# Performance work log

Hardware: AMD Instinct MI355X
Metric: run time of the kernel (lower is better)

## Reference

```python
import jax, jax.numpy as jnp
import numpy as np
import math

B, S, H, NH = 1, 2048, 1024, 16  # batch, seq, hidden, heads


def setup_inputs() -> dict:
    key = jax.random.key(0)
    ks = jax.random.split(key, 12)
    inp = {
        "query": jax.random.normal(ks[0], (B, S, H), dtype=jnp.float32),
        "key": jax.random.normal(ks[1], (B, S, H), dtype=jnp.float32),
        "value": jax.random.normal(ks[2], (B, S, H), dtype=jnp.float32),
        "attention_mask": jax.random.randint(ks[3], (1, 1, S, S), 0, 2, dtype=jnp.int32),
        # torch nn.Linear params: y = x @ W.T + b, W init ~ U(-1/sqrt(H), 1/sqrt(H))
        "Wq": jax.random.uniform(ks[4], (H, H), jnp.float32, -1, 1) / math.sqrt(H),
        "bq": jax.random.uniform(ks[5], (H,), jnp.float32, -1, 1) / math.sqrt(H),
        "Wk": jax.random.uniform(ks[6], (H, H), jnp.float32, -1, 1) / math.sqrt(H),
        "bk": jax.random.uniform(ks[7], (H,), jnp.float32, -1, 1) / math.sqrt(H),
        "Wv": jax.random.uniform(ks[8], (H, H), jnp.float32, -1, 1) / math.sqrt(H),
        "bv": jax.random.uniform(ks[9], (H,), jnp.float32, -1, 1) / math.sqrt(H),
        "Wo": jax.random.uniform(ks[10], (H, H), jnp.float32, -1, 1) / math.sqrt(H),
        "bo": jax.random.uniform(ks[11], (H,), jnp.float32, -1, 1) / math.sqrt(H),
        "head": NH,
        "hidden_size": H,
    }
    return inp


def reference(query, key, value, attention_mask, Wq, bq, Wk, bk, Wv, bv, Wo, bo, head, hidden_size):
    b, s, _ = query.shape
    d_k = hidden_size // head

    def proj(x, W, bias):
        # [b, s, hidden] -> [b, head, s, d_k]
        y = x @ W.T + bias
        return y.reshape(b, s, head, d_k).transpose(0, 2, 1, 3)

    q = proj(query, Wq, bq)
    k = proj(key, Wk, bk)
    v = proj(value, Wv, bv)

    # naive full score matrix, as in the source (scale by sqrt(d_k) = last dim of q)
    scores = jnp.einsum("bhqd,bhkd->bhqk", q, k) / math.sqrt(d_k)
    # faithful quirk: masked positions are set to 0 (not -inf) before softmax
    scores = jnp.where(attention_mask == 0, jnp.zeros((), scores.dtype), scores)
    attn = jax.nn.softmax(scores, axis=-1)

    out = jnp.einsum("bhqk,bhkd->bhqd", attn, v)  # [b, head, s, d_k]
    out = out.transpose(0, 2, 1, 3).reshape(b, s, head * d_k)
    return out @ Wo.T + bo
```

## Files before the change

kernel.cpp:

```cpp
#include <hip/hip_runtime.h>
#include <hip/hip_bf16.h>


#define S_LEN 2048
#define HID   1024
#define NHEAD 16
#define DK    64

typedef unsigned short u16;
typedef __attribute__((ext_vector_type(8))) short bf16x8;
typedef __attribute__((ext_vector_type(4))) short bf16x4;
typedef __attribute__((ext_vector_type(4))) float f32x4;

__device__ __forceinline__ void load16_lds(const void* g, void* l) {
  __builtin_amdgcn_global_load_lds(
      (const __attribute__((address_space(1))) void*)g,
      (__attribute__((address_space(3))) void*)l, 16, 0, 0);
}

__device__ __forceinline__ short bfbits(float x) {
  __hip_bfloat16 h = __float2bfloat16(x);
  return *(short*)&h;
}
__device__ __forceinline__ bf16x8 cvt8(float4 a, float4 b) {
  bf16x8 r;
  r[0] = bfbits(a.x); r[1] = bfbits(a.y); r[2] = bfbits(a.z); r[3] = bfbits(a.w);
  r[4] = bfbits(b.x); r[5] = bfbits(b.y); r[6] = bfbits(b.z); r[7] = bfbits(b.w);
  return r;
}
__device__ __forceinline__ float bf2f(u16 u) {
  unsigned v = (unsigned)u << 16;
  return *(float*)&v;
}

__global__ __launch_bounds__(256) void cvtW_kernel(
    const float* __restrict__ wq, const float* __restrict__ wk,
    const float* __restrict__ wv, const float* __restrict__ wo,
    u16* __restrict__ Wbf) {
  const int y = blockIdx.y;
  const float* src = y == 0 ? wq : (y == 1 ? wk : (y == 2 ? wv : wo));
  size_t i = ((size_t)blockIdx.x * 256 + threadIdx.x) * 8;
  float4 a = *(const float4*)(src + i);
  float4 b = *(const float4*)(src + i + 4);
  *(bf16x8*)(Wbf + (size_t)y * (HID * HID) + i) = cvt8(a, b);
}

__global__ void pack_mask_kernel(const int* __restrict__ mask,
                                 unsigned int* __restrict__ bits) {
  int w = blockIdx.x * blockDim.x + threadIdx.x;
  const int4* p = (const int4*)(mask + (size_t)w * 32);
  unsigned word = 0;
#pragma unroll
  for (int i = 0; i < 8; ++i) {
    int4 v = p[i];
    word |= (unsigned)(v.x != 0) << (i * 4 + 0);
    word |= (unsigned)(v.y != 0) << (i * 4 + 1);
    word |= (unsigned)(v.z != 0) << (i * 4 + 2);
    word |= (unsigned)(v.w != 0) << (i * 4 + 3);
  }
  bits[w] = word;
}

template <int BM, bool ABF>
__global__ __launch_bounds__(256) void gemm_bt(
    const void* A0, const void* A1, const void* A2,
    const u16* __restrict__ Wbase,
    const float* b0, const float* b1, const float* b2,
    void* C0, void* C1, void* C2,
    int store_fp32, int transpose_z2, int qscale_z0) {
  constexpr int Mm = 2048, Nn = 1024, Kk = 1024, BK = 64;
  constexpr int NIT = Kk / BK;
  constexpr int MT = BM / 32;
  constexpr int MTILES = Mm / BM;
  constexpr int AG = BM / 16;
  constexpr int AU = 2 * AG / 4;

  const int z = blockIdx.z;
  const void* A    = z == 0 ? A0 : (z == 1 ? A1 : A2);
  const u16*  W    = Wbase + (size_t)z * (Nn * Kk);
  const float* bias = z == 0 ? b0 : (z == 1 ? b1 : b2);
  void*       C    = z == 0 ? C0 : (z == 1 ? C1 : C2);
  const int transpose = (z == 2) ? transpose_z2 : 0;
  const float oscale = (z == 0 && qscale_z0) ? 0.125f : 1.0f;

  const int tid = threadIdx.x, lane = tid & 63, wave = tid >> 6;
  const int q4 = lane >> 4, c16 = lane & 15;
  const int bLin = blockIdx.x + blockIdx.y * gridDim.x;
  const int mBase = (bLin & (MTILES - 1)) * BM;
  const int nBase = (bLin / MTILES) * 128;
  const int wm = (wave >> 1) * (BM / 2), wn = (wave & 1) * 64;

  __shared__ __align__(16) u16 As[2][2][BM * 32];
  __shared__ __align__(16) u16 Bs[2][2][128 * 32];

  f32x4 acc[MT][4] = {};

  const int srow = lane >> 2;
  const int se8  = (lane & 3) * 8;

  const u16*   Ab = (const u16*)A;
  const float* Af = (const float*)A;

  auto issueW = [&](int it, int buf) {
#pragma unroll
    for (int j = 0; j < 4; ++j) {
      int i = wave * 4 + j;
      int h = i >> 3, grp = i & 7;
      load16_lds(W + (size_t)(nBase + grp * 16 + srow) * Kk + it * BK +
                     h * 32 + se8,
                 &Bs[buf][h][grp * 512]);
    }
  };
  auto issueA = [&](int it, int buf) {
#pragma unroll
    for (int j = 0; j < AU; ++j) {
      int i = wave * AU + j;
      int h = i / AG, grp = i % AG;
      load16_lds(Ab + (size_t)(mBase + grp * 16 + srow) * Kk + it * BK +
                     h * 32 + se8,
                 &As[buf][h][grp * 512]);
    }
  };
  float4 ar[AU][2];
  auto loadA = [&](int it) {
#pragma unroll
    for (int j = 0; j < AU; ++j) {
      int i = wave * AU + j;
      int h = i / AG, grp = i % AG;
      const float* s = Af + (size_t)(mBase + grp * 16 + srow) * Kk + it * BK +
                       h * 32 + se8;
      ar[j][0] = *(const float4*)s;
      ar[j][1] = *(const float4*)(s + 4);
    }
  };
  auto storeA = [&](int buf) {
#pragma unroll
    for (int j = 0; j < AU; ++j) {
      int i = wave * AU + j;
      int h = i / AG, grp = i % AG;
      *(bf16x8*)&As[buf][h][grp * 512 + srow * 32 + se8] =
          cvt8(ar[j][0], ar[j][1]);
    }
  };

  issueW(0, 0);
  if (ABF) {
    issueA(0, 0);
  } else {
    loadA(0);
    storeA(0);
  }
  __syncthreads();

  for (int it = 0; it < NIT; ++it) {
    const int buf = it & 1, nbuf = buf ^ 1;
    if (it + 1 < NIT) {
      issueW(it + 1, nbuf);
      if (ABF) issueA(it + 1, nbuf);
      else     loadA(it + 1);
    }
#pragma unroll
    for (int kk = 0; kk < 2; ++kk) {
      bf16x8 af[MT], bfr[4];
#pragma unroll
      for (int t = 0; t < MT; ++t)
        af[t] = *(const bf16x8*)&As[buf][kk][(wm + t * 16 + c16) * 32 + q4 * 8];
#pragma unroll
      for (int t = 0; t < 4; ++t)
        bfr[t] = *(const bf16x8*)&Bs[buf][kk][(wn + t * 16 + c16) * 32 + q4 * 8];
#pragma unroll
      for (int mt = 0; mt < MT; ++mt)
#pragma unroll
        for (int nt = 0; nt < 4; ++nt)
          acc[mt][nt] = __builtin_amdgcn_mfma_f32_16x16x32_bf16(
              af[mt], bfr[nt], acc[mt][nt], 0, 0, 0);
    }
    if (!ABF && it + 1 < NIT) storeA(nbuf);
    __syncthreads();
  }

#pragma unroll
  for (int nt = 0; nt < 4; ++nt) {
    int col = nBase + wn + nt * 16 + c16;
    float bv = bias[col];
#pragma unroll
    for (int mt = 0; mt < MT; ++mt) {
#pragma unroll
      for (int r = 0; r < 4; ++r) {
        int row = mBase + wm + mt * 16 + q4 * 4 + r;
        float v = (acc[mt][nt][r] + bv) * oscale;
        if (store_fp32)
          ((float*)C)[(size_t)row * Nn + col] = v;
        else if (transpose)
          ((__hip_bfloat16*)C)[(size_t)col * Mm + row] = __float2bfloat16(v);
        else
          ((__hip_bfloat16*)C)[(size_t)row * Nn + col] = __float2bfloat16(v);
      }
    }
  }
}

__global__ __launch_bounds__(256) void attn_kernel(
    const u16* __restrict__ Qb, const u16* __restrict__ Kb,
    const u16* __restrict__ Vt, const unsigned* __restrict__ mbits,
    u16* __restrict__ partO, float* __restrict__ partL) {
  constexpr int NITA = S_LEN / 2 / 64;
  const int qt = blockIdx.x, h = blockIdx.y, zz = blockIdx.z;
  const int tid = threadIdx.x, lane = tid & 63, wave = tid >> 6;
  const int q4 = lane >> 4, c16 = lane & 15;

  __shared__ __align__(16) u16 Ks[2][2][64 * 32];
  __shared__ __align__(16) u16 Vs[2][2][64 * 32];
  __shared__ __align__(16) u16 Ps[4][2 * 16 * 72];

  const int wq0 = qt * 128 + wave * 32;

  bf16x8 qf[2][2];
#pragma unroll
  for (int t = 0; t < 2; ++t)
#pragma unroll
    for (int kk = 0; kk < 2; ++kk)
      qf[t][kk] = *(const bf16x8*)(Qb + (size_t)(wq0 + t * 16 + c16) * HID +
                                   h * DK + kk * 32 + q4 * 8);

  f32x4 o[2][4] = {};
  float l_lane[2][4] = {};

  const int srow = lane >> 2;
  const int se8  = (lane & 3) * 8;
  const int kvbase = zz * (S_LEN / 2);

  auto issueKV = [&](int it, int buf) {
    const int kv0 = kvbase + it * 64;
#pragma unroll
    for (int j = 0; j < 2; ++j) {
      int ch = wave * 2 + j;
      int half = ch >> 2, grp = ch & 3;
      load16_lds(Kb + (size_t)(kv0 + grp * 16 + srow) * HID + h * DK +
                     half * 32 + se8,
                 &Ks[buf][half][grp * 512]);
      load16_lds(Vt + (size_t)(h * DK + grp * 16 + srow) * S_LEN + kv0 +
                     half * 32 + se8,
                 &Vs[buf][half][grp * 512]);
    }
  };

  issueKV(0, 0);
  __syncthreads();

  for (int it = 0; it < NITA; ++it) {
    const int buf = it & 1, nbuf = buf ^ 1;
    const int kv0 = kvbase + it * 64;
    if (it + 1 < NITA) issueKV(it + 1, nbuf);

    f32x4 sv[2][4];
#pragma unroll
    for (int nt = 0; nt < 4; ++nt) {
      bf16x8 kf0 = *(const bf16x8*)&Ks[buf][0][(nt * 16 + c16) * 32 + q4 * 8];
      bf16x8 kf1 = *(const bf16x8*)&Ks[buf][1][(nt * 16 + c16) * 32 + q4 * 8];
#pragma unroll
      for (int t = 0; t < 2; ++t) {
        f32x4 a = {};
        a = __builtin_amdgcn_mfma_f32_16x16x32_bf16(qf[t][0], kf0, a, 0, 0, 0);
        a = __builtin_amdgcn_mfma_f32_16x16x32_bf16(qf[t][1], kf1, a, 0, 0, 0);
        sv[t][nt] = a;
      }
    }

#pragma unroll
    for (int t = 0; t < 2; ++t)
#pragma unroll
      for (int r = 0; r < 4; ++r) {
        int row = wq0 + t * 16 + q4 * 4 + r;
        const unsigned* mrow = mbits + (size_t)row * 64 + (kv0 >> 5);
        unsigned w0 = mrow[0], w1 = mrow[1];
#pragma unroll
        for (int nt = 0; nt < 4; ++nt) {
          unsigned word = (nt < 2) ? w0 : w1;
          int bit = ((nt & 1) * 16) + c16;
          float s = ((word >> bit) & 1u) ? sv[t][nt][r] : 0.0f;
          float p = __expf(s);
          sv[t][nt][r] = p;
          l_lane[t][r] += p;
        }
      }

    u16* pw = &Ps[wave][0];
#pragma unroll
    for (int t = 0; t < 2; ++t)
#pragma unroll
      for (int r = 0; r < 4; ++r)
#pragma unroll
        for (int nt = 0; nt < 4; ++nt)
          ((__hip_bfloat16*)pw)[t * 1152 + (q4 * 4 + r) * 72 + nt * 16 + c16] =
              __float2bfloat16(sv[t][nt][r]);
    asm volatile("s_waitcnt lgkmcnt(0)" ::: "memory");

    bf16x8 vb[2][4];
#pragma unroll
    for (int kk = 0; kk < 2; ++kk)
#pragma unroll
      for (int nt = 0; nt < 4; ++nt)
        vb[kk][nt] =
            *(const bf16x8*)&Vs[buf][kk][(nt * 16 + c16) * 32 + q4 * 8];
#pragma unroll
    for (int t = 0; t < 2; ++t)
#pragma unroll
      for (int kk = 0; kk < 2; ++kk) {
        bf16x8 pa = *(const bf16x8*)&pw[t * 1152 + c16 * 72 + kk * 32 + q4 * 8];
#pragma unroll
        for (int nt = 0; nt < 4; ++nt)
          o[t][nt] = __builtin_amdgcn_mfma_f32_16x16x32_bf16(pa, vb[kk][nt],
                                                             o[t][nt], 0, 0, 0);
      }
    __syncthreads();
  }

#pragma unroll
  for (int t = 0; t < 2; ++t)
#pragma unroll
    for (int r = 0; r < 4; ++r) {
      float s = l_lane[t][r];
#pragma unroll
      for (int d = 1; d < 16; d <<= 1) s += __shfl_xor(s, d);
      l_lane[t][r] = s;
    }

#pragma unroll
  for (int t = 0; t < 2; ++t)
#pragma unroll
    for (int r = 0; r < 4; ++r) {
      int row = wq0 + t * 16 + q4 * 4 + r;
#pragma unroll
      for (int nt = 0; nt < 4; ++nt)
        ((__hip_bfloat16*)partO)[((size_t)zz * S_LEN + row) * HID + h * DK +
                                 nt * 16 + c16] = __float2bfloat16(o[t][nt][r]);
      if (c16 == 0)
        partL[((size_t)zz * NHEAD + h) * S_LEN + row] = l_lane[t][r];
    }
}

__global__ __launch_bounds__(256) void combine_kernel(
    const u16* __restrict__ partO, const float* __restrict__ partL,
    u16* __restrict__ ctx) {
  size_t idx = ((size_t)blockIdx.x * 256 + threadIdx.x) * 4;
  int row = (int)(idx >> 10);
  int col = (int)(idx & 1023);
  int h = col >> 6;
  float l = partL[(size_t)h * S_LEN + row] +
            partL[((size_t)NHEAD + h) * S_LEN + row];
  float inv = 1.0f / l;
  bf16x4 a = *(const bf16x4*)(partO + idx);
  bf16x4 b = *(const bf16x4*)(partO + (size_t)S_LEN * HID + idx);
  bf16x4 r;
#pragma unroll
  for (int j = 0; j < 4; ++j) {
    float v = (bf2f((u16)a[j]) + bf2f((u16)b[j])) * inv;
    r[j] = bfbits(v);
  }
  *(bf16x4*)(ctx + idx) = r;
}

extern "C" void kernel_launch(void* const* d_in, const int* in_sizes, int n_in,
                              void* d_out, int out_size, void* d_ws, size_t ws_size,
                              hipStream_t stream) {
  const float* q    = (const float*)d_in[0];
  const float* k    = (const float*)d_in[1];
  const float* v    = (const float*)d_in[2];
  const int*   mask = (const int*)d_in[3];
  const float* Wq = (const float*)d_in[4];
  const float* bq = (const float*)d_in[5];
  const float* Wk = (const float*)d_in[6];
  const float* bk = (const float*)d_in[7];
  const float* Wv = (const float*)d_in[8];
  const float* bv = (const float*)d_in[9];
  const float* Wo = (const float*)d_in[10];
  const float* bo = (const float*)d_in[11];

  const size_t M2 = (size_t)S_LEN * HID;
  const size_t need = (4 + 2 + 2 + 2 + 2) * M2 * 2 +
                      (size_t)S_LEN * 64 * 4 + 2 * NHEAD * S_LEN * 4;
  if (ws_size < need) return;

  u16* Wbf   = (u16*)d_ws;
  u16* partO = Wbf + 4 * (size_t)HID * HID / 2 * 2;
  u16* Qb    = partO + 2 * M2;
  u16* Kb    = Qb + M2;
  u16* Vt    = Kb + M2;
  unsigned* mbits = (unsigned*)(Vt + M2);
  float* partL = (float*)(mbits + (size_t)S_LEN * 64);
  u16* ctx = Qb;

  hipLaunchKernelGGL(cvtW_kernel, dim3(512, 4), dim3(256), 0, stream,
                     Wq, Wk, Wv, Wo, Wbf);

  hipLaunchKernelGGL(pack_mask_kernel, dim3((S_LEN * (S_LEN / 32)) / 256),
                     dim3(256), 0, stream, mask, mbits);

  hipLaunchKernelGGL((gemm_bt<128, false>), dim3(8, 16, 3), dim3(256), 0,
                     stream, q, k, v, Wbf, bq, bk, bv,
                     (void*)Qb, (void*)Kb, (void*)Vt, 0, 1, 1);

  hipLaunchKernelGGL(attn_kernel, dim3(S_LEN / 128, NHEAD, 2), dim3(256), 0,
                     stream, Qb, Kb, Vt, mbits, partO, partL);

  hipLaunchKernelGGL(combine_kernel, dim3((S_LEN * HID / 4) / 256), dim3(256),
                     0, stream, partO, partL, ctx);

  hipLaunchKernelGGL((gemm_bt<64, true>), dim3(8, 32, 1), dim3(256), 0,
                     stream, ctx, ctx, ctx, Wbf + 3 * (size_t)HID * HID,
                     bo, bo, bo, d_out, d_out, d_out, 1, 0, 0);
}
```

Measured before the change: 222.8 us.

## Double waves per block in GEMM and attention kernels, shrinking per-wave tiles

Both GEMM kernels and the attention kernel now launch 512 threads (8 waves) instead of 256. In the GEMM each wave computes a narrower 32-column slice, and the tile loads are spread over more waves. In attention each wave owns 16 query rows instead of 32, and K and V loads are split between the two halves of the waves. The aim is more waves in flight to hide latency and fewer registers per wave. The cost is that each wave reuses its loaded fragments less, so LDS reads per MFMA go up.

Result: faster. 213.5 us (-4.2%).

```diff
diff --git a/kernel.cpp b/kernel.cpp
--- a/kernel.cpp
+++ b/kernel.cpp
@@ -62,7 +62,7 @@
 }
 
 template <int BM, bool ABF>
-__global__ __launch_bounds__(256) void gemm_bt(
+__global__ __launch_bounds__(512) void gemm_bt(
     const void* A0, const void* A1, const void* A2,
     const u16* __restrict__ Wbase,
     const float* b0, const float* b1, const float* b2,
@@ -73,7 +73,7 @@
   constexpr int MT = BM / 32;
   constexpr int MTILES = Mm / BM;
   constexpr int AG = BM / 16;
-  constexpr int AU = 2 * AG / 4;
+  constexpr int AU = BM / 64;
 
   const int z = blockIdx.z;
   const void* A    = z == 0 ? A0 : (z == 1 ? A1 : A2);
@@ -86,14 +86,14 @@
   const int tid = threadIdx.x, lane = tid & 63, wave = tid >> 6;
   const int q4 = lane >> 4, c16 = lane & 15;
   const int bLin = blockIdx.x + blockIdx.y * gridDim.x;
-  const int mBase = (bLin & (MTILES - 1)) * BM;
+  const int mBase = (bLin % MTILES) * BM;
   const int nBase = (bLin / MTILES) * 128;
-  const int wm = (wave >> 1) * (BM / 2), wn = (wave & 1) * 64;
+  const int wm = (wave >> 2) * (BM / 2), wn = (wave & 3) * 32;
 
   __shared__ __align__(16) u16 As[2][2][BM * 32];
   __shared__ __align__(16) u16 Bs[2][2][128 * 32];
 
-  f32x4 acc[MT][4] = {};
+  f32x4 acc[MT][2] = {};
 
   const int srow = lane >> 2;
   const int se8  = (lane & 3) * 8;
@@ -103,9 +103,9 @@
 
   auto issueW = [&](int it, int buf) {
 #pragma unroll
-    for (int j = 0; j < 4; ++j) {
-      int i = wave * 4 + j;
-      int h = i >> 3, grp = i & 7;
+    for (int j = 0; j < 2; ++j) {
+      int u = wave * 2 + j;
+      int h = u >> 3, grp = u & 7;
       load16_lds(W + (size_t)(nBase + grp * 16 + srow) * Kk + it * BK +
                      h * 32 + se8,
                  &Bs[buf][h][grp * 512]);
@@ -114,8 +114,8 @@
   auto issueA = [&](int it, int buf) {
 #pragma unroll
     for (int j = 0; j < AU; ++j) {
-      int i = wave * AU + j;
-      int h = i / AG, grp = i % AG;
+      int u = wave * AU + j;
+      int h = u / AG, grp = u % AG;
       load16_lds(Ab + (size_t)(mBase + grp * 16 + srow) * Kk + it * BK +
                      h * 32 + se8,
                  &As[buf][h][grp * 512]);
@@ -125,8 +125,8 @@
   auto loadA = [&](int it) {
 #pragma unroll
     for (int j = 0; j < AU; ++j) {
-      int i = wave * AU + j;
-      int h = i / AG, grp = i % AG;
+      int u = wave * AU + j;
+      int h = u / AG, grp = u % AG;
       const float* s = Af + (size_t)(mBase + grp * 16 + srow) * Kk + it * BK +
                        h * 32 + se8;
       ar[j][0] = *(const float4*)s;
@@ -136,20 +136,16 @@
   auto storeA = [&](int buf) {
 #pragma unroll
     for (int j = 0; j < AU; ++j) {
-      int i = wave * AU + j;
-      int h = i / AG, grp = i % AG;
+      int u = wave * AU + j;
+      int h = u / AG, grp = u % AG;
       *(bf16x8*)&As[buf][h][grp * 512 + srow * 32 + se8] =
           cvt8(ar[j][0], ar[j][1]);
     }
   };
 
   issueW(0, 0);
-  if (ABF) {
-    issueA(0, 0);
-  } else {
-    loadA(0);
-    storeA(0);
-  }
+  if (ABF) issueA(0, 0);
+  else { loadA(0); storeA(0); }
   __syncthreads();
 
   for (int it = 0; it < NIT; ++it) {
@@ -161,17 +157,17 @@
     }
 #pragma unroll
     for (int kk = 0; kk < 2; ++kk) {
-      bf16x8 af[MT], bfr[4];
+      bf16x8 af[MT], bfr[2];
 #pragma unroll
       for (int t = 0; t < MT; ++t)
         af[t] = *(const bf16x8*)&As[buf][kk][(wm + t * 16 + c16) * 32 + q4 * 8];
 #pragma unroll
-      for (int t = 0; t < 4; ++t)
+      for (int t = 0; t < 2; ++t)
         bfr[t] = *(const bf16x8*)&Bs[buf][kk][(wn + t * 16 + c16) * 32 + q4 * 8];
 #pragma unroll
       for (int mt = 0; mt < MT; ++mt)
 #pragma unroll
-        for (int nt = 0; nt < 4; ++nt)
+        for (int nt = 0; nt < 2; ++nt)
           acc[mt][nt] = __builtin_amdgcn_mfma_f32_16x16x32_bf16(
               af[mt], bfr[nt], acc[mt][nt], 0, 0, 0);
     }
@@ -180,7 +176,7 @@
   }
 
 #pragma unroll
-  for (int nt = 0; nt < 4; ++nt) {
+  for (int nt = 0; nt < 2; ++nt) {
     int col = nBase + wn + nt * 16 + c16;
     float bv = bias[col];
 #pragma unroll
@@ -200,7 +196,7 @@
   }
 }
 
-__global__ __launch_bounds__(256) void attn_kernel(
+__global__ __launch_bounds__(512) void attn_kernel(
     const u16* __restrict__ Qb, const u16* __restrict__ Kb,
     const u16* __restrict__ Vt, const unsigned* __restrict__ mbits,
     u16* __restrict__ partO, float* __restrict__ partL) {
@@ -211,20 +207,18 @@
 
   __shared__ __align__(16) u16 Ks[2][2][64 * 32];
   __shared__ __align__(16) u16 Vs[2][2][64 * 32];
-  __shared__ __align__(16) u16 Ps[4][2 * 16 * 72];
-
-  const int wq0 = qt * 128 + wave * 32;
-
-  bf16x8 qf[2][2];
-#pragma unroll
-  for (int t = 0; t < 2; ++t)
-#pragma unroll
-    for (int kk = 0; kk < 2; ++kk)
-      qf[t][kk] = *(const bf16x8*)(Qb + (size_t)(wq0 + t * 16 + c16) * HID +
-                                   h * DK + kk * 32 + q4 * 8);
-
-  f32x4 o[2][4] = {};
-  float l_lane[2][4] = {};
+  __shared__ __align__(16) u16 Ps[8][16 * 72];
+
+  const int wq0 = qt * 128 + wave * 16;
+
+  bf16x8 qf[2];
+#pragma unroll
+  for (int kk = 0; kk < 2; ++kk)
+    qf[kk] = *(const bf16x8*)(Qb + (size_t)(wq0 + c16) * HID + h * DK +
+                              kk * 32 + q4 * 8);
+
+  f32x4 o[4] = {};
+  float l_lane[4] = {};
 
   const int srow = lane >> 2;
   const int se8  = (lane & 3) * 8;
@@ -234,14 +228,19 @@
     const int kv0 = kvbase + it * 64;
 #pragma unroll
     for (int j = 0; j < 2; ++j) {
-      int ch = wave * 2 + j;
-      int half = ch >> 2, grp = ch & 3;
-      load16_lds(Kb + (size_t)(kv0 + grp * 16 + srow) * HID + h * DK +
-                     half * 32 + se8,
-                 &Ks[buf][half][grp * 512]);
-      load16_lds(Vt + (size_t)(h * DK + grp * 16 + srow) * S_LEN + kv0 +
-                     half * 32 + se8,
-                 &Vs[buf][half][grp * 512]);
+      int i = wave * 2 + j;
+      if (i < 8) {
+        int half = i >> 2, grp = i & 3;
+        load16_lds(Kb + (size_t)(kv0 + grp * 16 + srow) * HID + h * DK +
+                       half * 32 + se8,
+                   &Ks[buf][half][grp * 512]);
+      } else {
+        int ii = i - 8;
+        int half = ii >> 2, grp = ii & 3;
+        load16_lds(Vt + (size_t)(h * DK + grp * 16 + srow) * S_LEN + kv0 +
+                       half * 32 + se8,
+                   &Vs[buf][half][grp * 512]);
+      }
     }
   };
 
@@ -253,91 +252,72 @@
     const int kv0 = kvbase + it * 64;
     if (it + 1 < NITA) issueKV(it + 1, nbuf);
 
-    f32x4 sv[2][4];
+    f32x4 sv[4];
 #pragma unroll
     for (int nt = 0; nt < 4; ++nt) {
       bf16x8 kf0 = *(const bf16x8*)&Ks[buf][0][(nt * 16 + c16) * 32 + q4 * 8];
       bf16x8 kf1 = *(const bf16x8*)&Ks[buf][1][(nt * 16 + c16) * 32 + q4 * 8];
-#pragma unroll
-      for (int t = 0; t < 2; ++t) {
-        f32x4 a = {};
-        a = __builtin_amdgcn_mfma_f32_16x16x32_bf16(qf[t][0], kf0, a, 0, 0, 0);
-        a = __builtin_amdgcn_mfma_f32_16x16x32_bf16(qf[t][1], kf1, a, 0, 0, 0);
-        sv[t][nt] = a;
+      f32x4 a = {};
+      a = __builtin_amdgcn_mfma_f32_16x16x32_bf16(qf[0], kf0, a, 0, 0, 0);
+      a = __builtin_amdgcn_mfma_f32_16x16x32_bf16(qf[1], kf1, a, 0, 0, 0);
+      sv[nt] = a;
+    }
+
+#pragma unroll
+    for (int r = 0; r < 4; ++r) {
+      int row = wq0 + q4 * 4 + r;
+      const unsigned* mrow = mbits + (size_t)row * 64 + (kv0 >> 5);
+      unsigned w0 = mrow[0], w1 = mrow[1];
+#pragma unroll
+      for (int nt = 0; nt < 4; ++nt) {
+        unsigned word = (nt < 2) ? w0 : w1;
+        int bit = ((nt & 1) * 16) + c16;
+        float s = ((word >> bit) & 1u) ? sv[nt][r] : 0.0f;
+        float p = __expf(s);
+        sv[nt][r] = p;
+        l_lane[r] += p;
       }
     }
 
-#pragma unroll
-    for (int t = 0; t < 2; ++t)
-#pragma unroll
-      for (int r = 0; r < 4; ++r) {
-        int row = wq0 + t * 16 + q4 * 4 + r;
-        const unsigned* mrow = mbits + (size_t)row * 64 + (kv0 >> 5);
-        unsigned w0 = mrow[0], w1 = mrow[1];
-#pragma unroll
-        for (int nt = 0; nt < 4; ++nt) {
-          unsigned word = (nt < 2) ? w0 : w1;
-          int bit = ((nt & 1) * 16) + c16;
-          float s = ((word >> bit) & 1u) ? sv[t][nt][r] : 0.0f;
-          float p = __expf(s);
-          sv[t][nt][r] = p;
-          l_lane[t][r] += p;
-        }
+    u16* pw = &Ps[wave][0];
+#pragma unroll
+    for (int r = 0; r < 4; ++r)
+#pragma unroll
+      for (int nt = 0; nt < 4; ++nt)
+        ((__hip_bfloat16*)pw)[(q4 * 4 + r) * 72 + nt * 16 + c16] =
+            __float2bfloat16(sv[nt][r]);
+    asm volatile("s_waitcnt lgkmcnt(0)" ::: "memory");
+
+#pragma unroll
+    for (int kk = 0; kk < 2; ++kk) {
+      bf16x8 pa = *(const bf16x8*)&pw[c16 * 72 + kk * 32 + q4 * 8];
+#pragma unroll
+      for (int nt = 0; nt < 4; ++nt) {
+        bf16x8 vb = *(const bf16x8*)&Vs[buf][kk][(nt * 16 + c16) * 32 + q4 * 8];
+        o[nt] = __builtin_amdgcn_mfma_f32_16x16x32_bf16(pa, vb, o[nt], 0, 0, 0);
       }
-
-    u16* pw = &Ps[wave][0];
-#pragma unroll
-    for (int t = 0; t < 2; ++t)
-#pragma unroll
-      for (int r = 0; r < 4; ++r)
-#pragma unroll
-        for (int nt = 0; nt < 4; ++nt)
-          ((__hip_bfloat16*)pw)[t * 1152 + (q4 * 4 + r) * 72 + nt * 16 + c16] =
-              __float2bfloat16(sv[t][nt][r]);
-    asm volatile("s_waitcnt lgkmcnt(0)" ::: "memory");
-
-    bf16x8 vb[2][4];
-#pragma unroll
-    for (int kk = 0; kk < 2; ++kk)
-#pragma unroll
-      for (int nt = 0; nt < 4; ++nt)
-        vb[kk][nt] =
-            *(const bf16x8*)&Vs[buf][kk][(nt * 16 + c16) * 32 + q4 * 8];
-#pragma unroll
-    for (int t = 0; t < 2; ++t)
-#pragma unroll
-      for (int kk = 0; kk < 2; ++kk) {
-        bf16x8 pa = *(const bf16x8*)&pw[t * 1152 + c16 * 72 + kk * 32 + q4 * 8];
-#pragma unroll
-        for (int nt = 0; nt < 4; ++nt)
-          o[t][nt] = __builtin_amdgcn_mfma_f32_16x16x32_bf16(pa, vb[kk][nt],
-                                                             o[t][nt], 0, 0, 0);
-      }
+    }
     __syncthreads();
   }
 
 #pragma unroll
-  for (int t = 0; t < 2; ++t)
-#pragma unroll
-    for (int r = 0; r < 4; ++r) {
-      float s = l_lane[t][r];
-#pragma unroll
-      for (int d = 1; d < 16; d <<= 1) s += __shfl_xor(s, d);
-      l_lane[t][r] = s;
-    }
-
-#pragma unroll
-  for (int t = 0; t < 2; ++t)
-#pragma unroll
-    for (int r = 0; r < 4; ++r) {
-      int row = wq0 + t * 16 + q4 * 4 + r;
-#pragma unroll
-      for (int nt = 0; nt < 4; ++nt)
-        ((__hip_bfloat16*)partO)[((size_t)zz * S_LEN + row) * HID + h * DK +
-                                 nt * 16 + c16] = __float2bfloat16(o[t][nt][r]);
-      if (c16 == 0)
-        partL[((size_t)zz * NHEAD + h) * S_LEN + row] = l_lane[t][r];
-    }
+  for (int r = 0; r < 4; ++r) {
+    float s = l_lane[r];
+#pragma unroll
+    for (int d = 1; d < 16; d <<= 1) s += __shfl_xor(s, d);
+    l_lane[r] = s;
+  }
+
+#pragma unroll
+  for (int r = 0; r < 4; ++r) {
+    int row = wq0 + q4 * 4 + r;
+#pragma unroll
+    for (int nt = 0; nt < 4; ++nt)
+      ((__hip_bfloat16*)partO)[((size_t)zz * S_LEN + row) * HID + h * DK +
+                               nt * 16 + c16] = __float2bfloat16(o[nt][r]);
+    if (c16 == 0)
+      partL[((size_t)zz * NHEAD + h) * S_LEN + row] = l_lane[r];
+  }
 }
 
 __global__ __launch_bounds__(256) void combine_kernel(
@@ -397,17 +377,17 @@
   hipLaunchKernelGGL(pack_mask_kernel, dim3((S_LEN * (S_LEN / 32)) / 256),
                      dim3(256), 0, stream, mask, mbits);
 
-  hipLaunchKernelGGL((gemm_bt<128, false>), dim3(8, 16, 3), dim3(256), 0,
+  hipLaunchKernelGGL((gemm_bt<128, false>), dim3(8, 16, 3), dim3(512), 0,
                      stream, q, k, v, Wbf, bq, bk, bv,
                      (void*)Qb, (void*)Kb, (void*)Vt, 0, 1, 1);
 
-  hipLaunchKernelGGL(attn_kernel, dim3(S_LEN / 128, NHEAD, 2), dim3(256), 0,
+  hipLaunchKernelGGL(attn_kernel, dim3(S_LEN / 128, NHEAD, 2), dim3(512), 0,
                      stream, Qb, Kb, Vt, mbits, partO, partL);
 
   hipLaunchKernelGGL(combine_kernel, dim3((S_LEN * HID / 4) / 256), dim3(256),
                      0, stream, partO, partL, ctx);
 
-  hipLaunchKernelGGL((gemm_bt<64, true>), dim3(8, 32, 1), dim3(256), 0,
+  hipLaunchKernelGGL((gemm_bt<64, true>), dim3(8, 32, 1), dim3(512), 0,
                      stream, ctx, ctx, ctx, Wbf + 3 * (size_t)HID * HID,
                      bo, bo, bo, d_out, d_out, d_out, 1, 0, 0);
 }
```
